# Kernel optimization log

Measured on AMD Instinct MI355X. Metric: run time of the kernel, lower is better.

The kernel has to match this reference:

```python
import jax, jax.numpy as jnp
import numpy as np

B, L, D = 2, 2048, 2048
H, HKV, HD = 32, 8, 64
G = H // HKV  # GQA group size


def _rope(t, cos, sin):
    # t: [B, h, L, HD]; cos/sin: [L, HD//2]; pairs are consecutive (view_as_complex)
    tr, ti = t[..., 0::2], t[..., 1::2]
    out_r = tr * cos - ti * sin
    out_i = tr * sin + ti * cos
    return jnp.stack([out_r, out_i], axis=-1).reshape(t.shape)


def setup_inputs() -> dict:
    key = jax.random.key(0)
    ks = jax.random.split(key, 5)
    x = jax.random.normal(ks[0], (B, L, D), dtype=jnp.float32)
    wq = jax.random.normal(ks[1], (D, H * HD), dtype=jnp.float32) * 0.02
    wk = jax.random.normal(ks[2], (D, HKV * HD), dtype=jnp.float32) * 0.02
    wv = jax.random.normal(ks[3], (D, HKV * HD), dtype=jnp.float32) * 0.02
    wo = jax.random.normal(ks[4], (D, D), dtype=jnp.float32) * 0.02
    # RoPE freqs: theta_i = 10000^(-2i/HD), angle[p, i] = p * theta_i
    inv_freq = 1.0 / (10000.0 ** (jnp.arange(0, HD, 2, dtype=jnp.float32) / HD))
    angles = jnp.arange(L, dtype=jnp.float32)[:, None] * inv_freq[None, :]  # [L, HD//2]
    freqs_cos = jnp.cos(angles)
    freqs_sin = jnp.sin(angles)
    # additive causal mask [L, L]
    mask = jnp.where(jnp.tril(jnp.ones((L, L), dtype=bool)), 0.0, -1e9).astype(jnp.float32)
    return {"x": x, "wq": wq, "wk": wk, "wv": wv, "wo": wo,
            "freqs_cos": freqs_cos, "freqs_sin": freqs_sin, "mask": mask}


def reference(x, wq, wk, wv, wo, freqs_cos, freqs_sin, mask):
    b, l, _ = x.shape
    q = (x @ wq).reshape(b, l, H, HD).transpose(0, 2, 1, 3)      # [B, H, L, HD]
    k = (x @ wk).reshape(b, l, HKV, HD).transpose(0, 2, 1, 3)    # [B, HKV, L, HD]
    v = (x @ wv).reshape(b, l, HKV, HD).transpose(0, 2, 1, 3)
    q = _rope(q, freqs_cos, freqs_sin)
    k = _rope(k, freqs_cos, freqs_sin)
    # native GQA broadcast instead of repeat_kv copy (same math)
    qg = q.reshape(b, HKV, G, l, HD)
    scores = jnp.einsum("bhgqd,bhkd->bhgqk", qg, k) / jnp.sqrt(jnp.float32(HD))
    scores = scores + mask  # [B, HKV, G, L, L]
    probs = jax.nn.softmax(scores.astype(jnp.float32), axis=-1).astype(v.dtype)
    out = jnp.einsum("bhgqk,bhkd->bhgqd", probs, v)              # [B, HKV, G, L, HD]
    out = out.reshape(b, H, l, HD).transpose(0, 2, 1, 3).reshape(b, l, H * HD)
    return out @ wo
```

## Files before the change

kernel.cpp:

```cpp
#include <hip/hip_runtime.h>
#include <hip/hip_bf16.h>

#define B_   2
#define L_   2048
#define D_   2048
#define H_   32
#define HKV_ 8
#define HD_  64
#define G_   4
#define M_   4096
#define NF_  3072

typedef __attribute__((ext_vector_type(8))) short bf16x8;
typedef __attribute__((ext_vector_type(4))) float f32x4;

static __device__ __forceinline__ unsigned short f2bf(float f) {
  unsigned int u = __float_as_uint(f);
  unsigned int r = (u + 0x7FFFu + ((u >> 16) & 1u)) >> 16;
  return (unsigned short)r;
}
static __device__ __forceinline__ unsigned short f2bf_hw(float f) {
  __hip_bfloat16 h = __float2bfloat16(f);
  return *(unsigned short*)&h;
}

#define GLD16(g, l) __builtin_amdgcn_global_load_lds(                      \
    (const __attribute__((address_space(1))) void*)(g),                    \
    (__attribute__((address_space(3))) void*)(l), 16, 0, 0)

__global__ void cast_bf16_kernel(const float* __restrict__ in,
                                 unsigned short* __restrict__ out, int n4) {
  int i = blockIdx.x * blockDim.x + threadIdx.x;
  if (i >= n4) return;
  float4 v = ((const float4*)in)[i];
  uint2 r;
  r.x = (unsigned int)f2bf(v.x) | ((unsigned int)f2bf(v.y) << 16);
  r.y = (unsigned int)f2bf(v.z) | ((unsigned int)f2bf(v.w) << 16);
  ((uint2*)out)[i] = r;
}

__global__ void transpose_cast_kernel(const float* __restrict__ src,
                                      unsigned short* __restrict__ dst,
                                      int K, int N) {
  __shared__ float tile[32][33];
  int k0 = blockIdx.y * 32, n0 = blockIdx.x * 32;
  int tx = threadIdx.x, ty = threadIdx.y;
#pragma unroll
  for (int r = 0; r < 4; ++r)
    tile[ty * 4 + r][tx] = src[(size_t)(k0 + ty * 4 + r) * N + n0 + tx];
  __syncthreads();
#pragma unroll
  for (int r = 0; r < 4; ++r)
    dst[(size_t)(n0 + ty * 4 + r) * K + k0 + tx] = f2bf(tile[tx][ty * 4 + r]);
}

__global__ __launch_bounds__(256)
void gemm_bt_kernel(const unsigned short* __restrict__ A,
                    const unsigned short* __restrict__ Bt,
                    float* __restrict__ C, int M, int N, int K) {
  __shared__ unsigned short Al[128 * 32];
  __shared__ unsigned short Bl[128 * 32];
  const int tid = threadIdx.x;
  const int w = tid >> 6;
  const int l = tid & 63;
  const int row0 = blockIdx.y * 128;
  const int col0 = blockIdx.x * 128;
  const int wr = (w >> 1) * 64, wc = (w & 1) * 64;

  f32x4 acc[4][4];
#pragma unroll
  for (int m = 0; m < 4; ++m)
#pragma unroll
    for (int n = 0; n < 4; ++n) acc[m][n] = (f32x4){0.f, 0.f, 0.f, 0.f};

  const int srow = l >> 2;
  const int scol = (l & 3) * 8;
  const int fr = l & 15, fk = (l >> 4) * 8;
  const int nk = K / 32;

  for (int kt = 0; kt < nk; ++kt) {
    const int k0 = kt * 32;
#pragma unroll
    for (int t = 0; t < 2; ++t) {
      const int rr = (w * 2 + t) * 16 + srow;
      GLD16(A + (size_t)(row0 + rr) * K + k0 + scol, &Al[(w * 2 + t) * 512]);
      GLD16(Bt + (size_t)(col0 + rr) * K + k0 + scol, &Bl[(w * 2 + t) * 512]);
    }
    __syncthreads();
    bf16x8 af[4], bfr[4];
#pragma unroll
    for (int m = 0; m < 4; ++m)
      af[m] = *(const bf16x8*)&Al[(wr + m * 16 + fr) * 32 + fk];
#pragma unroll
    for (int n = 0; n < 4; ++n)
      bfr[n] = *(const bf16x8*)&Bl[(wc + n * 16 + fr) * 32 + fk];
#pragma unroll
    for (int m = 0; m < 4; ++m)
#pragma unroll
      for (int n = 0; n < 4; ++n)
        acc[m][n] = __builtin_amdgcn_mfma_f32_16x16x32_bf16(af[m], bfr[n], acc[m][n], 0, 0, 0);
    __syncthreads();
  }

  const int fq = l >> 4;
#pragma unroll
  for (int m = 0; m < 4; ++m)
#pragma unroll
    for (int n = 0; n < 4; ++n)
#pragma unroll
      for (int j = 0; j < 4; ++j) {
        int r = row0 + wr + m * 16 + fq * 4 + j;
        int c = col0 + wc + n * 16 + fr;
        C[(size_t)r * N + c] = acc[m][n][j];
      }
}

__global__ void rope_kernel(const float* __restrict__ src,
                            const float* __restrict__ cosf,
                            const float* __restrict__ sinf,
                            unsigned short* __restrict__ dst, int nh, int col_off,
                            float scale, int total) {
  int idx = blockIdx.x * blockDim.x + threadIdx.x;
  if (idx >= total) return;
  int i = idx & 31;
  int h = (idx >> 5) & (nh - 1);
  int row = idx / (nh << 5);
  int lpos = row & (L_ - 1);
  int b = row >> 11;
  const float* s = src + (size_t)row * NF_ + col_off + h * 64 + 2 * i;
  float tr = s[0], ti = s[1];
  float c = cosf[lpos * 32 + i], sn = sinf[lpos * 32 + i];
  float orr = (tr * c - ti * sn) * scale;
  float oii = (tr * sn + ti * c) * scale;
  size_t o = (((size_t)(b * nh + h)) * L_ + lpos) * 64 + 2 * i;
  unsigned int packed = (unsigned int)f2bf(orr) | ((unsigned int)f2bf(oii) << 16);
  *(unsigned int*)&dst[o] = packed;
}

__global__ void cast_vT_kernel(const float* __restrict__ v,
                               unsigned short* __restrict__ vT) {
  __shared__ float tile[32][33];
  int l0 = blockIdx.x * 32, d0 = blockIdx.y * 32;
  int z = blockIdx.z;
  int b = z >> 3, hkv = z & 7;
  int tx = threadIdx.x, ty = threadIdx.y;
  const float* src = v + (size_t)(b * L_) * NF_ + 2560 + hkv * 64;
#pragma unroll
  for (int r = 0; r < 4; ++r)
    tile[ty * 4 + r][tx] = src[(size_t)(l0 + ty * 4 + r) * NF_ + d0 + tx];
  __syncthreads();
  unsigned short* dst = vT + ((size_t)z * 64) * L_;
#pragma unroll
  for (int r = 0; r < 4; ++r)
    dst[(size_t)(d0 + ty * 4 + r) * L_ + l0 + tx] = f2bf(tile[tx][ty * 4 + r]);
}

__global__ __launch_bounds__(256)
void attn_kernel(const unsigned short* __restrict__ Q,
                 const unsigned short* __restrict__ Kt,
                 const unsigned short* __restrict__ Vt,
                 unsigned short* __restrict__ O) {
  __shared__ unsigned short Kl[64 * 64];
  __shared__ unsigned short Vl[64 * 64];
  __shared__ unsigned short Pl[64 * 64];
  const int tid = threadIdx.x, w = tid >> 6, l = tid & 63;
  const int bh = blockIdx.x;
  const int b = bh >> 5, h = bh & 31;
  const int hkv = h >> 2;
  const int pair = blockIdx.y;
  const int fr = l & 15, hi = l >> 4;
  const int frx = fr & 7;

  const int srow = l >> 3;
  const int scole = ((l & 7) ^ srow) * 8;

  const unsigned short* kbase = Kt + ((size_t)(b * HKV_ + hkv)) * L_ * 64;
  const unsigned short* vbase = Vt + ((size_t)(b * HKV_ + hkv)) * 64 * L_;

  for (int half = 0; half < 2; ++half) {
    const int by = half ? (15 - pair) : pair;
    const int q0 = by * 128;

    bf16x8 qf[2][2];
#pragma unroll
    for (int s = 0; s < 2; ++s) {
      const unsigned short* qb =
          Q + (((size_t)bh) * L_ + q0 + s * 64 + w * 16 + fr) * 64 + hi * 8;
      qf[s][0] = *(const bf16x8*)(qb);
      qf[s][1] = *(const bf16x8*)(qb + 32);
    }

    float m_i[2][4], l_p[2][4];
    f32x4 oacc[2][4];
#pragma unroll
    for (int s = 0; s < 2; ++s)
#pragma unroll
      for (int j = 0; j < 4; ++j) { m_i[s][j] = -1e30f; l_p[s][j] = 0.f; }
#pragma unroll
    for (int s = 0; s < 2; ++s)
#pragma unroll
      for (int nf = 0; nf < 4; ++nf) oacc[s][nf] = (f32x4){0.f, 0.f, 0.f, 0.f};

    const int nt = 2 * by + 2;

    for (int t = 0; t < nt; ++t) {
      const int kv0 = t * 64;
#pragma unroll
      for (int u = 0; u < 2; ++u) {
        const int c = w * 2 + u;
        const int rr = c * 8 + srow;
        GLD16(kbase + ((size_t)(kv0 + rr)) * 64 + scole, &Kl[c * 512]);
        GLD16(vbase + ((size_t)rr) * L_ + kv0 + scole, &Vl[c * 512]);
      }
      __syncthreads();

#pragma unroll
      for (int s = 0; s < 2; ++s) {
        const int dlim = 2 * by + s;
        if (t > dlim) continue;

        f32x4 sacc[4];
#pragma unroll
        for (int nf = 0; nf < 4; ++nf) sacc[nf] = (f32x4){0.f, 0.f, 0.f, 0.f};
#pragma unroll
        for (int ks = 0; ks < 2; ++ks) {
#pragma unroll
          for (int nf = 0; nf < 4; ++nf) {
            bf16x8 kfrag = *(const bf16x8*)
                &Kl[(nf * 16 + fr) * 64 + (((ks * 4 + hi) ^ frx) * 8)];
            sacc[nf] = __builtin_amdgcn_mfma_f32_16x16x32_bf16(qf[s][ks], kfrag, sacc[nf], 0, 0, 0);
          }
        }

        if (t == dlim) {
          const int rbase = q0 + s * 64 + w * 16 + hi * 4;
#pragma unroll
          for (int nf = 0; nf < 4; ++nf)
#pragma unroll
            for (int j = 0; j < 4; ++j)
              if (kv0 + nf * 16 + fr > rbase + j) sacc[nf][j] = -1e30f;
        }

        float rowmax[4];
#pragma unroll
        for (int j = 0; j < 4; ++j) {
          float mx = fmaxf(fmaxf(sacc[0][j], sacc[1][j]),
                           fmaxf(sacc[2][j], sacc[3][j]));
          mx = fmaxf(mx, __shfl_xor(mx, 1));
          mx = fmaxf(mx, __shfl_xor(mx, 2));
          mx = fmaxf(mx, __shfl_xor(mx, 4));
          mx = fmaxf(mx, __shfl_xor(mx, 8));
          rowmax[j] = mx;
        }

        float g = rowmax[0] - m_i[s][0];
        g = fmaxf(g, rowmax[1] - m_i[s][1]);
        g = fmaxf(g, rowmax[2] - m_i[s][2]);
        g = fmaxf(g, rowmax[3] - m_i[s][3]);
        if (!__all(g <= 8.f)) {
#pragma unroll
          for (int j = 0; j < 4; ++j) {
            float mnew = fmaxf(m_i[s][j], rowmax[j]);
            float cr = exp2f(m_i[s][j] - mnew);
            m_i[s][j] = mnew;
            l_p[s][j] *= cr;
#pragma unroll
            for (int nf = 0; nf < 4; ++nf) oacc[s][nf][j] *= cr;
          }
        }

#pragma unroll
        for (int j = 0; j < 4; ++j) {
          const int prow = w * 16 + hi * 4 + j;
#pragma unroll
          for (int nf = 0; nf < 4; ++nf) {
            float p = exp2f(sacc[nf][j] - m_i[s][j]);
            l_p[s][j] += p;
            Pl[prow * 64 + (((nf * 2 + (fr >> 3)) ^ (prow & 7)) * 8) + frx] =
                f2bf_hw(p);
          }
        }

#pragma unroll
        for (int ks = 0; ks < 2; ++ks) {
          bf16x8 pa = *(const bf16x8*)
              &Pl[(w * 16 + fr) * 64 + (((ks * 4 + hi) ^ frx) * 8)];
#pragma unroll
          for (int nf = 0; nf < 4; ++nf) {
            bf16x8 vfrag = *(const bf16x8*)
                &Vl[(nf * 16 + fr) * 64 + (((ks * 4 + hi) ^ frx) * 8)];
            oacc[s][nf] = __builtin_amdgcn_mfma_f32_16x16x32_bf16(pa, vfrag, oacc[s][nf], 0, 0, 0);
          }
        }
      }
      __syncthreads();
    }

#pragma unroll
    for (int s = 0; s < 2; ++s)
#pragma unroll
      for (int j = 0; j < 4; ++j) {
        float lsum = l_p[s][j];
        lsum += __shfl_xor(lsum, 1);
        lsum += __shfl_xor(lsum, 2);
        lsum += __shfl_xor(lsum, 4);
        lsum += __shfl_xor(lsum, 8);
        float inv = 1.0f / lsum;
#pragma unroll
        for (int nf = 0; nf < 4; ++nf) {
          int qrow = q0 + s * 64 + w * 16 + hi * 4 + j;
          int d = nf * 16 + fr;
          O[((size_t)(b * L_ + qrow)) * 2048 + h * 64 + d] =
              f2bf_hw(oacc[s][nf][j] * inv);
        }
      }
  }
}

extern "C" void kernel_launch(void* const* d_in, const int* in_sizes, int n_in,
                              void* d_out, int out_size, void* d_ws, size_t ws_size,
                              hipStream_t stream) {
  (void)in_sizes; (void)n_in; (void)out_size; (void)ws_size;
  const float* x  = (const float*)d_in[0];
  const float* wq = (const float*)d_in[1];
  const float* wk = (const float*)d_in[2];
  const float* wv = (const float*)d_in[3];
  const float* wo = (const float*)d_in[4];
  const float* fc = (const float*)d_in[5];
  const float* fs = (const float*)d_in[6];
  float* out = (float*)d_out;

  char* ws = (char*)d_ws;
  unsigned short* x_b  = (unsigned short*)(ws + 0);
  unsigned short* wT   = (unsigned short*)(ws + 16777216);
  unsigned short* woT  = (unsigned short*)(ws + 29360128);
  float* qkv_f         = (float*)(ws + 37748736);
  unsigned short* at_b = (unsigned short*)(ws + 37748736);
  unsigned short* q_b  = (unsigned short*)(ws + 88080384);
  unsigned short* k_b  = (unsigned short*)(ws + 104857600);
  unsigned short* vT_b = (unsigned short*)(ws + 109051904);

  const float qscale = 0.125f * 1.4426950408889634f;

  dim3 tb(32, 8);
  cast_bf16_kernel<<<8192, 256, 0, stream>>>(x, x_b, M_ * D_ / 4);
  transpose_cast_kernel<<<dim3(64, 64), tb, 0, stream>>>(wq, wT, 2048, 2048);
  transpose_cast_kernel<<<dim3(16, 64), tb, 0, stream>>>(wk, wT + (size_t)2048 * 2048, 2048, 512);
  transpose_cast_kernel<<<dim3(16, 64), tb, 0, stream>>>(wv, wT + (size_t)2560 * 2048, 2048, 512);
  transpose_cast_kernel<<<dim3(64, 64), tb, 0, stream>>>(wo, woT, 2048, 2048);

  gemm_bt_kernel<<<dim3(24, 32), 256, 0, stream>>>(x_b, wT, qkv_f, M_, NF_, 2048);

  rope_kernel<<<16384, 256, 0, stream>>>(qkv_f, fc, fs, q_b, 32, 0, qscale, M_ * 32 * 32);
  rope_kernel<<<4096, 256, 0, stream>>>(qkv_f, fc, fs, k_b, 8, 2048, 1.0f, M_ * 8 * 32);
  cast_vT_kernel<<<dim3(64, 2, 16), tb, 0, stream>>>(qkv_f, vT_b);

  attn_kernel<<<dim3(64, 8), 256, 0, stream>>>(q_b, k_b, vT_b, at_b);

  gemm_bt_kernel<<<dim3(16, 32), 256, 0, stream>>>(at_b, woT, out, M_, 2048, 2048);
}
```

Measured before the change: 399.0 us.

## Replace GEMM with 256x256-tile double-buffered kernel and add MFMA priority hints

Both projection GEMMs move from a 128x128 tile with a single LDS buffer to a 256x256 tile. The new kernel uses 8 waves, a K-step of 64, a swizzled LDS layout, and a double-buffered prefetch of the next K tile interleaved with the MFMA phases. It also raises wave priority around the MFMA blocks in both the GEMM and attention kernels. The aim is more operand reuse per loaded byte and overlap of global loads with compute. The cost is 128KB of dynamic LDS and far fewer blocks: 12x16 for QKV and 8x16 for the output projection on 256 CUs. That can leave much of the GPU idle.

```diff
diff --git a/kernel.cpp b/kernel.cpp
--- a/kernel.cpp
+++ b/kernel.cpp
@@ -54,65 +54,115 @@
     dst[(size_t)(n0 + ty * 4 + r) * K + k0 + tx] = f2bf(tile[tx][ty * 4 + r]);
 }
 
-__global__ __launch_bounds__(256)
-void gemm_bt_kernel(const unsigned short* __restrict__ A,
+__global__ __launch_bounds__(512, 2)
+void gemm256_kernel(const unsigned short* __restrict__ A,
                     const unsigned short* __restrict__ Bt,
                     float* __restrict__ C, int M, int N, int K) {
-  __shared__ unsigned short Al[128 * 32];
-  __shared__ unsigned short Bl[128 * 32];
+  extern __shared__ unsigned short lds[];
   const int tid = threadIdx.x;
-  const int w = tid >> 6;
-  const int l = tid & 63;
-  const int row0 = blockIdx.y * 128;
-  const int col0 = blockIdx.x * 128;
-  const int wr = (w >> 1) * 64, wc = (w & 1) * 64;
-
-  f32x4 acc[4][4];
-#pragma unroll
-  for (int m = 0; m < 4; ++m)
+  const int w = tid >> 6, l = tid & 63;
+  const int wave_m = w >> 2, wave_n = w & 3;
+  const int fr = l & 15, hi = l >> 4;
+  const int row0 = blockIdx.y * 256, col0 = blockIdx.x * 256;
+  const int NT = K >> 6;
+
+  const int lr0 = w * 8 + (l >> 3);
+  const int lr1 = 64 + lr0;
+  const int sc0 = (((l & 7) ^ (((lr0 >> 2) & 1) << 1)) << 3);
+  const int sc1 = (((l & 7) ^ (((lr1 >> 2) & 1) << 1)) << 3);
+
+  const int sw = ((fr >> 2) & 1) << 4;
+
+  f32x4 acc[8][4];
+#pragma unroll
+  for (int m = 0; m < 8; ++m)
 #pragma unroll
     for (int n = 0; n < 4; ++n) acc[m][n] = (f32x4){0.f, 0.f, 0.f, 0.f};
 
-  const int srow = l >> 2;
-  const int scol = (l & 3) * 8;
-  const int fr = l & 15, fk = (l >> 4) * 8;
-  const int nk = K / 32;
-
-  for (int kt = 0; kt < nk; ++kt) {
-    const int k0 = kt * 32;
-#pragma unroll
-    for (int t = 0; t < 2; ++t) {
-      const int rr = (w * 2 + t) * 16 + srow;
-      GLD16(A + (size_t)(row0 + rr) * K + k0 + scol, &Al[(w * 2 + t) * 512]);
-      GLD16(Bt + (size_t)(col0 + rr) * K + k0 + scol, &Bl[(w * 2 + t) * 512]);
+#define STAGE_A(buf_, kt_) do {                                                \
+    const int base_ = (buf_) * 16384;                                          \
+    GLD16(A + (size_t)(row0 + lr0) * K + (kt_) * 64 + sc0,                     \
+          &lds[base_ + w * 512]);                                              \
+    GLD16(A + (size_t)(row0 + lr1) * K + (kt_) * 64 + sc1,                     \
+          &lds[base_ + (8 + w) * 512]);                                        \
+    GLD16(A + (size_t)(row0 + 128 + lr0) * K + (kt_) * 64 + sc0,               \
+          &lds[base_ + 8192 + w * 512]);                                       \
+    GLD16(A + (size_t)(row0 + 128 + lr1) * K + (kt_) * 64 + sc1,               \
+          &lds[base_ + 8192 + (8 + w) * 512]);                                 \
+  } while (0)
+#define STAGE_B(buf_, kt_) do {                                                \
+    const int base_ = 32768 + (buf_) * 16384;                                  \
+    GLD16(Bt + (size_t)(col0 + lr0) * K + (kt_) * 64 + sc0,                    \
+          &lds[base_ + w * 512]);                                              \
+    GLD16(Bt + (size_t)(col0 + lr1) * K + (kt_) * 64 + sc1,                    \
+          &lds[base_ + (8 + w) * 512]);                                        \
+    GLD16(Bt + (size_t)(col0 + 128 + lr0) * K + (kt_) * 64 + sc0,              \
+          &lds[base_ + 8192 + w * 512]);                                       \
+    GLD16(Bt + (size_t)(col0 + 128 + lr1) * K + (kt_) * 64 + sc1,              \
+          &lds[base_ + 8192 + (8 + w) * 512]);                                 \
+  } while (0)
+
+  STAGE_A(0, 0);
+  STAGE_B(0, 0);
+  asm volatile("s_waitcnt vmcnt(0)" ::: "memory");
+  __builtin_amdgcn_s_barrier();
+
+  bf16x8 bfrag[4][2];
+  const int brow = (wave_n & 1) * 64;
+
+  for (int kt = 0; kt < NT; ++kt) {
+    const int buf = kt & 1;
+    const int ab = buf * 16384 + wave_m * 8192;
+    const int bb = 32768 + buf * 16384 + (wave_n >> 1) * 8192 + brow * 64;
+#pragma unroll
+    for (int p = 0; p < 4; ++p) {
+      if (p == 0) {
+#pragma unroll
+        for (int nf = 0; nf < 4; ++nf)
+#pragma unroll
+          for (int kk = 0; kk < 2; ++kk)
+            bfrag[nf][kk] = *(const bf16x8*)
+                &lds[bb + (nf * 16 + fr) * 64 + ((kk * 32 + hi * 8) ^ sw)];
+      }
+      bf16x8 afrag[2][2];
+#pragma unroll
+      for (int mi = 0; mi < 2; ++mi)
+#pragma unroll
+        for (int kk = 0; kk < 2; ++kk)
+          afrag[mi][kk] = *(const bf16x8*)
+              &lds[ab + ((p * 2 + mi) * 16 + fr) * 64 + ((kk * 32 + hi * 8) ^ sw)];
+      if (kt + 1 < NT) {
+        if (p == 0) STAGE_A(buf ^ 1, kt + 1);
+        else if (p == 1) STAGE_B(buf ^ 1, kt + 1);
+      }
+      __builtin_amdgcn_s_barrier();
+      __builtin_amdgcn_s_setprio(1);
+#pragma unroll
+      for (int mi = 0; mi < 2; ++mi)
+#pragma unroll
+        for (int nf = 0; nf < 4; ++nf)
+#pragma unroll
+          for (int kk = 0; kk < 2; ++kk)
+            acc[p * 2 + mi][nf] = __builtin_amdgcn_mfma_f32_16x16x32_bf16(
+                afrag[mi][kk], bfrag[nf][kk], acc[p * 2 + mi][nf], 0, 0, 0);
+      __builtin_amdgcn_s_setprio(0);
+      if (p == 3) asm volatile("s_waitcnt vmcnt(0)" ::: "memory");
+      __builtin_amdgcn_s_barrier();
     }
-    __syncthreads();
-    bf16x8 af[4], bfr[4];
-#pragma unroll
-    for (int m = 0; m < 4; ++m)
-      af[m] = *(const bf16x8*)&Al[(wr + m * 16 + fr) * 32 + fk];
+  }
+
+#pragma unroll
+  for (int m = 0; m < 8; ++m)
 #pragma unroll
     for (int n = 0; n < 4; ++n)
-      bfr[n] = *(const bf16x8*)&Bl[(wc + n * 16 + fr) * 32 + fk];
-#pragma unroll
-    for (int m = 0; m < 4; ++m)
-#pragma unroll
-      for (int n = 0; n < 4; ++n)
-        acc[m][n] = __builtin_amdgcn_mfma_f32_16x16x32_bf16(af[m], bfr[n], acc[m][n], 0, 0, 0);
-    __syncthreads();
-  }
-
-  const int fq = l >> 4;
-#pragma unroll
-  for (int m = 0; m < 4; ++m)
-#pragma unroll
-    for (int n = 0; n < 4; ++n)
 #pragma unroll
       for (int j = 0; j < 4; ++j) {
-        int r = row0 + wr + m * 16 + fq * 4 + j;
-        int c = col0 + wc + n * 16 + fr;
+        int r = row0 + wave_m * 128 + m * 16 + hi * 4 + j;
+        int c = col0 + wave_n * 64 + n * 16 + fr;
         C[(size_t)r * N + c] = acc[m][n][j];
       }
+#undef STAGE_A
+#undef STAGE_B
 }
 
 __global__ void rope_kernel(const float* __restrict__ src,
@@ -222,6 +272,7 @@
         f32x4 sacc[4];
 #pragma unroll
         for (int nf = 0; nf < 4; ++nf) sacc[nf] = (f32x4){0.f, 0.f, 0.f, 0.f};
+        __builtin_amdgcn_s_setprio(1);
 #pragma unroll
         for (int ks = 0; ks < 2; ++ks) {
 #pragma unroll
@@ -231,6 +282,7 @@
             sacc[nf] = __builtin_amdgcn_mfma_f32_16x16x32_bf16(qf[s][ks], kfrag, sacc[nf], 0, 0, 0);
           }
         }
+        __builtin_amdgcn_s_setprio(0);
 
         if (t == dlim) {
           const int rbase = q0 + s * 64 + w * 16 + hi * 4;
@@ -281,6 +333,7 @@
           }
         }
 
+        __builtin_amdgcn_s_setprio(1);
 #pragma unroll
         for (int ks = 0; ks < 2; ++ks) {
           bf16x8 pa = *(const bf16x8*)
@@ -292,6 +345,7 @@
             oacc[s][nf] = __builtin_amdgcn_mfma_f32_16x16x32_bf16(pa, vfrag, oacc[s][nf], 0, 0, 0);
           }
         }
+        __builtin_amdgcn_s_setprio(0);
       }
       __syncthreads();
     }
@@ -342,6 +396,9 @@
 
   const float qscale = 0.125f * 1.4426950408889634f;
 
+  hipFuncSetAttribute((const void*)gemm256_kernel,
+                      hipFuncAttributeMaxDynamicSharedMemorySize, 131072);
+
   dim3 tb(32, 8);
   cast_bf16_kernel<<<8192, 256, 0, stream>>>(x, x_b, M_ * D_ / 4);
   transpose_cast_kernel<<<dim3(64, 64), tb, 0, stream>>>(wq, wT, 2048, 2048);
@@ -349,7 +406,8 @@
   transpose_cast_kernel<<<dim3(16, 64), tb, 0, stream>>>(wv, wT + (size_t)2560 * 2048, 2048, 512);
   transpose_cast_kernel<<<dim3(64, 64), tb, 0, stream>>>(wo, woT, 2048, 2048);
 
-  gemm_bt_kernel<<<dim3(24, 32), 256, 0, stream>>>(x_b, wT, qkv_f, M_, NF_, 2048);
+  gemm256_kernel<<<dim3(NF_ / 256, M_ / 256), 512, 131072, stream>>>(
+      x_b, wT, qkv_f, M_, NF_, 2048);
 
   rope_kernel<<<16384, 256, 0, stream>>>(qkv_f, fc, fs, q_b, 32, 0, qscale, M_ * 32 * 32);
   rope_kernel<<<4096, 256, 0, stream>>>(qkv_f, fc, fs, k_b, 8, 2048, 1.0f, M_ * 8 * 32);
@@ -357,5 +415,6 @@
 
   attn_kernel<<<dim3(64, 8), 256, 0, stream>>>(q_b, k_b, vT_b, at_b);
 
-  gemm_bt_kernel<<<dim3(16, 32), 256, 0, stream>>>(at_b, woT, out, M_, 2048, 2048);
-}
+  gemm256_kernel<<<dim3(2048 / 256, M_ / 256), 512, 131072, stream>>>(
+      at_b, woT, out, M_, 2048, 2048);
+}
```

Measured after the change: 404.8 us. About the same (+1.4%).
